# Performance work log

Measured on AMD Instinct MI355X. Metric: run time of the kernel, lower is better.

Reference implementation:

```python
import jax, jax.numpy as jnp
import numpy as np

DIM = 1024
HEADS = 16
DIM_HEAD = 64
INNER = HEADS * DIM_HEAD  # 1024
SCALE = DIM ** (-0.5)  # module scales by dim**-0.5 (not dim_head)


def setup_inputs() -> dict:
    key = jax.random.key(0)
    kx, kqkv, kwo, kbo = jax.random.split(key, 4)
    x = jax.random.normal(kx, (2, 2048, DIM), dtype=jnp.float32)
    W_qkv = jax.random.normal(kqkv, (DIM, 3 * INNER), dtype=jnp.float32) * (DIM ** -0.5)
    W_out = jax.random.normal(kwo, (INNER, DIM), dtype=jnp.float32) * (INNER ** -0.5)
    b_out = jax.random.normal(kbo, (DIM,), dtype=jnp.float32) * 0.01
    return {"x": x, "W_qkv": W_qkv, "W_out": W_out, "b_out": b_out}


def reference(x, W_qkv, W_out, b_out):
    b, n, _ = x.shape
    qkv = x @ W_qkv  # [b, n, 3*inner]
    q, k, v = jnp.split(qkv, 3, axis=-1)
    # [b, n, h*d] -> [b, h, n, d]
    reshape = lambda t: t.reshape(b, n, HEADS, DIM_HEAD).transpose(0, 2, 1, 3)
    q, k, v = reshape(q), reshape(k), reshape(v)
    dots = jnp.einsum('bhid,bhjd->bhij', q, k) * SCALE  # [b, h, n, n]
    attn = jax.nn.softmax(dots, axis=-1)
    out = jnp.einsum('bhij,bhjd->bhid', attn, v)  # [b, h, n, d]
    out = out.transpose(0, 2, 1, 3).reshape(b, n, INNER)
    return out @ W_out + b_out
```

## Files before the change

### kernel.cpp

```cpp
#include <hip/hip_runtime.h>

typedef __bf16 bf16x8 __attribute__((ext_vector_type(8)));
typedef __bf16 bf16x4 __attribute__((ext_vector_type(4)));
typedef __bf16 bf16x2 __attribute__((ext_vector_type(2)));
typedef float f32x4 __attribute__((ext_vector_type(4)));
typedef float f32x16 __attribute__((ext_vector_type(16)));
typedef int i32x4 __attribute__((ext_vector_type(4)));
typedef unsigned int u32x2 __attribute__((ext_vector_type(2)));

__device__ __forceinline__ void async16(void* lds, const void* g) {
  __builtin_amdgcn_global_load_lds(
      (__attribute__((address_space(1))) unsigned int*)(g),
      (__attribute__((address_space(3))) unsigned int*)(lds), 16, 0, 0);
}

__device__ __forceinline__ unsigned int pack2(float a, float b) {
  bf16x2 t;
  t[0] = (__bf16)a;
  t[1] = (__bf16)b;
  return __builtin_bit_cast(unsigned int, t);
}

__device__ __forceinline__ void plswap(unsigned int& d, unsigned int& s) {
#if __has_builtin(__builtin_amdgcn_permlane32_swap)
  u32x2 r = __builtin_amdgcn_permlane32_swap(d, s, false, false);
  d = r[0];
  s = r[1];
#else
  asm("v_permlane32_swap_b32 %0, %1" : "+v"(d), "+v"(s));
#endif
}

__device__ __forceinline__ int detect_block(const unsigned short* win, int* cnt_sh) {
  if (threadIdx.x == 0) *cnt_sh = 0;
  __syncthreads();
  int c = 0;
#pragma unroll
  for (int j = 0; j < 8; j++) {
    const unsigned short u = win[threadIdx.x * 8 + j];
    if (((u >> 7) & 0xFF) >= 0xC0) c++;
  }
  if (c) atomicAdd(cnt_sh, c);
  __syncthreads();
  return (*cnt_sh >= 64) ? 1 : 0;
}

__global__ __launch_bounds__(256) void prep(
    const void* __restrict__ x, const void* __restrict__ Wqkv,
    const void* __restrict__ Wout, __bf16* __restrict__ xb,
    __bf16* __restrict__ WqkvT, __bf16* __restrict__ WoutT,
    int* __restrict__ flagp)
{
  __shared__ __bf16 tile[64 * 65];
  __shared__ int cnt;
  const int bx = blockIdx.x;
  const int t = threadIdx.x;

  if (bx < 2048) {
    const long base = (long)bx * 2048;
    const int f = detect_block((const unsigned short*)x + base, &cnt);
    if (bx == 0 && t == 0) *flagp = f;
    const long i = base + t * 8;
    if (f) {
      const float* s = (const float*)x;
#pragma unroll
      for (int j = 0; j < 8; j++) xb[i + j] = (__bf16)s[i + j];
    } else {
      *(bf16x8*)&xb[i] = *(const bf16x8*)((const __bf16*)x + i);
    }
    return;
  }

  const void* in;  __bf16* out;  int R = 1024, C, tcx, tr;
  if (bx < 2816) {
    const int idx = bx - 2048;
    in = Wqkv; out = WqkvT; C = 3072; tcx = (idx % 48) * 64; tr = (idx / 48) * 64;
  } else {
    const int idx = bx - 2816;
    in = Wout; out = WoutT; C = 1024; tcx = (idx % 16) * 64; tr = (idx / 16) * 64;
  }
  const int f = detect_block((const unsigned short*)in + (long)tr * C + tcx, &cnt);
#pragma unroll
  for (int i = 0; i < 16; i++) {
    const int idx = t + 256 * i;
    const int r = idx >> 6, c = idx & 63;
    const long g = (long)(tr + r) * C + tcx + c;
    tile[r * 65 + c] = f ? (__bf16)((const float*)in)[g] : ((const __bf16*)in)[g];
  }
  __syncthreads();
#pragma unroll
  for (int i = 0; i < 16; i++) {
    const int idx = t + 256 * i;
    const int r = idx >> 6, c = idx & 63;
    out[(long)(tcx + r) * R + tr + c] = tile[c * 65 + r];
  }
}

__global__ __launch_bounds__(256, 3) void gemm_qkv(
    const __bf16* __restrict__ A, const __bf16* __restrict__ Bt,
    __bf16* __restrict__ Cqk, __bf16* __restrict__ Vt)
{
  __shared__ __bf16 smem[17408];
  const int t = threadIdx.x;
  const int l = t & 63;
  const int w = t >> 6;
  const int wr = w >> 1, wc = w & 1;
  const long m0 = (long)blockIdx.x * 128;
  const long n0 = (long)blockIdx.y * 128;
  const int K = 1024;

  const int srow = w * 16 + (l >> 2);
  const int skof = (l & 3) * 8;
  const __bf16* gA = A + (m0 + srow) * (long)K + skof;
  const __bf16* gB = Bt + (n0 + srow) * (long)K + skof;
  const int Ao[2] = {0, 8192}, Bo[2] = {4096, 12288};
  const int lof = w * 512 + l * 8;

  async16(smem + Ao[0] + lof,        gA);
  async16(smem + Ao[0] + 2048 + lof, gA + 64 * (long)K);
  async16(smem + Bo[0] + lof,        gB);
  async16(smem + Bo[0] + 2048 + lof, gB + 64 * (long)K);
  gA += 32; gB += 32;
  __syncthreads();

  f32x4 acc[4][4] = {};

  for (int it = 0; it < 32; it++) {
    if (it < 31) {
      const int nb = (it + 1) & 1;
      async16(smem + Ao[nb] + lof,        gA);
      async16(smem + Ao[nb] + 2048 + lof, gA + 64 * (long)K);
      async16(smem + Bo[nb] + lof,        gB);
      async16(smem + Bo[nb] + 2048 + lof, gB + 64 * (long)K);
      gA += 32; gB += 32;
    }
    const __bf16* As = smem + Ao[it & 1];
    const __bf16* Bs = smem + Bo[it & 1];
    bf16x8 af[4], bfr[4];
#pragma unroll
    for (int mi = 0; mi < 4; mi++)
      af[mi] = *(const bf16x8*)&As[(wr * 64 + mi * 16 + (l & 15)) * 32 + (l >> 4) * 8];
#pragma unroll
    for (int ni = 0; ni < 4; ni++)
      bfr[ni] = *(const bf16x8*)&Bs[(wc * 64 + ni * 16 + (l & 15)) * 32 + (l >> 4) * 8];
#pragma unroll
    for (int mi = 0; mi < 4; mi++)
#pragma unroll
      for (int ni = 0; ni < 4; ni++)
        acc[mi][ni] = __builtin_amdgcn_mfma_f32_16x16x32_bf16(af[mi], bfr[ni], acc[mi][ni], 0, 0, 0);
    __syncthreads();
  }

  if (n0 < 2048) {
#pragma unroll
    for (int mi = 0; mi < 4; mi++)
#pragma unroll
      for (int ni = 0; ni < 4; ni++) {
        const long col = n0 + wc * 64 + ni * 16 + (l & 15);
#pragma unroll
        for (int r = 0; r < 4; r++) {
          const long row = m0 + wr * 64 + mi * 16 + (l >> 4) * 4 + r;
          Cqk[row * 2048 + col] = (__bf16)acc[mi][ni][r];
        }
      }
  } else {
#pragma unroll
    for (int mi = 0; mi < 4; mi++)
#pragma unroll
      for (int ni = 0; ni < 4; ni++) {
        const int c = wc * 64 + ni * 16 + (l & 15);
        const int r = wr * 64 + mi * 16 + (l >> 4) * 4;
        bf16x4 pk;
#pragma unroll
        for (int k = 0; k < 4; k++) pk[k] = (__bf16)acc[mi][ni][k];
        *(bf16x4*)&smem[c * 136 + r] = pk;
      }
    __syncthreads();
    const int b = (int)(m0 >> 11);
    const int nbase = (int)(m0 & 2047);
#pragma unroll
    for (int i = 0; i < 8; i++) {
      const int c = (t >> 4) + i * 16;
      const int r8 = (t & 15) * 8;
      const bf16x8 v = *(const bf16x8*)&smem[c * 136 + r8];
      const int vcol = (int)(n0 - 2048) + c;
      *(bf16x8*)&Vt[((long)(b * 16 + (vcol >> 6)) * 64 + (vcol & 63)) * 2048 + nbase + r8] = v;
    }
  }
}

__global__ __launch_bounds__(256, 2) void gemm_out(
    const __bf16* __restrict__ A, const __bf16* __restrict__ Bt,
    const void* __restrict__ bias_raw, void* __restrict__ C,
    const int* __restrict__ flagp)
{
  __shared__ __bf16 smem[12288];
  const int t = threadIdx.x;
  const int l = t & 63;
  const int w = t >> 6;
  const int wr = w >> 1, wc = w & 1;
  const long m0 = (long)blockIdx.x * 128;
  const long n0 = (long)blockIdx.y * 64;
  const int of = *flagp;
  const int K = 1024;

  const int srow = w * 16 + (l >> 2);
  const int skof = (l & 3) * 8;
  const __bf16* gA = A + (m0 + srow) * (long)K + skof;
  const __bf16* gB = Bt + (n0 + srow) * (long)K + skof;
  const int Ao[2] = {0, 6144}, Bo[2] = {4096, 10240};
  const int lof = w * 512 + l * 8;

  async16(smem + Ao[0] + lof,        gA);
  async16(smem + Ao[0] + 2048 + lof, gA + 64 * (long)K);
  async16(smem + Bo[0] + lof,        gB);
  gA += 32; gB += 32;
  __syncthreads();

  f32x4 acc[4][2] = {};

  for (int it = 0; it < 32; it++) {
    if (it < 31) {
      const int nb = (it + 1) & 1;
      async16(smem + Ao[nb] + lof,        gA);
      async16(smem + Ao[nb] + 2048 + lof, gA + 64 * (long)K);
      async16(smem + Bo[nb] + lof,        gB);
      gA += 32; gB += 32;
    }
    const __bf16* As = smem + Ao[it & 1];
    const __bf16* Bs = smem + Bo[it & 1];
    bf16x8 af[4], bfr[2];
#pragma unroll
    for (int mi = 0; mi < 4; mi++)
      af[mi] = *(const bf16x8*)&As[(wr * 64 + mi * 16 + (l & 15)) * 32 + (l >> 4) * 8];
#pragma unroll
    for (int ni = 0; ni < 2; ni++)
      bfr[ni] = *(const bf16x8*)&Bs[(wc * 32 + ni * 16 + (l & 15)) * 32 + (l >> 4) * 8];
#pragma unroll
    for (int mi = 0; mi < 4; mi++)
#pragma unroll
      for (int ni = 0; ni < 2; ni++)
        acc[mi][ni] = __builtin_amdgcn_mfma_f32_16x16x32_bf16(af[mi], bfr[ni], acc[mi][ni], 0, 0, 0);
    __syncthreads();
  }

#pragma unroll
  for (int mi = 0; mi < 4; mi++)
#pragma unroll
    for (int ni = 0; ni < 2; ni++) {
      const long col = n0 + wc * 32 + ni * 16 + (l & 15);
      const float bv = of ? ((const float*)bias_raw)[col]
                          : (float)((const __bf16*)bias_raw)[col];
#pragma unroll
      for (int r = 0; r < 4; r++) {
        const long row = m0 + wr * 64 + mi * 16 + (l >> 4) * 4 + r;
        const float val = acc[mi][ni][r] + bv;
        const long off = row * 1024 + col;
        if (of) ((float*)C)[off] = val;
        else    ((__bf16*)C)[off] = (__bf16)val;
      }
    }
}

#define EXP2_SCALE 0.045084439f

__global__ __launch_bounds__(256, 4) void attn_kernel(
    const __bf16* __restrict__ qk, const __bf16* __restrict__ Vt,
    __bf16* __restrict__ O)
{
  __shared__ __bf16 smem[16384];
  const int t = threadIdx.x;
  const int l = t & 63;
  const int w = t >> 6;
  const int wi = w & 1, wj = w >> 1;
  const int hl = l >> 5;
  const int i7 = l & 7;
  const int L = blockIdx.y * 32 + blockIdx.x;
  const int bh = (L & 7) * 4 + ((L >> 3) & 3);
  const int qt = L >> 5;
  const int b = bh >> 4, head = bh & 15;
  const long q_row0 = (long)b * 2048 + qt * 64;

  const int srow = w * 8 + (l >> 3);
  const int sdof = ((l & 7) ^ (l >> 3)) * 8;
  const int lof = w * 512 + l * 8;

  const __bf16* gK = qk + ((long)b * 2048 + srow) * 2048 + 1024 + head * 64 + sdof;
  const __bf16* gV = Vt + ((long)bh * 64 + srow) * 2048 + sdof;
  async16(smem + lof,        gK);
  async16(smem + 2048 + lof, gK + 32 * 2048);
  async16(smem + 4096 + lof, gV);
  async16(smem + 6144 + lof, gV + 32 * 2048);
  gK += (long)64 * 2048;
  gV += 64;

  bf16x8 qf[4];
  {
    const __bf16* gQ = qk + (q_row0 + wi * 32 + (l & 31)) * 2048 + head * 64 + hl * 8;
#pragma unroll
    for (int kc = 0; kc < 4; kc++)
      qf[kc] = *(const bf16x8*)(gQ + kc * 16);
  }

  f32x16 accA = {0,0,0,0,0,0,0,0,0,0,0,0,0,0,0,0};
  f32x16 accB = {0,0,0,0,0,0,0,0,0,0,0,0,0,0,0,0};
  float l_i = 0.0f;

  for (int it = 0; it < 32; it++) {
    __syncthreads();
    if (it < 31) {
      const int nb = ((it + 1) & 1) * 8192;
      async16(smem + nb + lof,        gK);
      async16(smem + nb + 2048 + lof, gK + 32 * 2048);
      async16(smem + nb + 4096 + lof, gV);
      async16(smem + nb + 6144 + lof, gV + 32 * 2048);
      gK += (long)64 * 2048;
      gV += 64;
    }
    const __bf16* Ks = smem + (it & 1) * 8192;
    const __bf16* Vs = Ks + 4096;

    f32x16 st = {0,0,0,0,0,0,0,0,0,0,0,0,0,0,0,0};
    __builtin_amdgcn_s_setprio(1);
#pragma unroll
    for (int kc = 0; kc < 4; kc++) {
      const bf16x8 ak = *(const bf16x8*)&Ks[(wj * 32 + (l & 31)) * 64 + (((kc * 2 + hl) ^ i7) * 8)];
      st = __builtin_amdgcn_mfma_f32_32x32x16_bf16(ak, qf[kc], st, 0, 0, 0);
    }
    __builtin_amdgcn_s_setprio(0);

    float rs = 0.0f;
#pragma unroll
    for (int r = 0; r < 16; r++) {
      const float p = exp2f(st[r] * EXP2_SCALE);
      st[r] = p;
      rs += p;
    }
    rs += __shfl_xor(rs, 32, 64);
    l_i += rs;

    unsigned int a0 = pack2(st[0],  st[1]),  b0 = pack2(st[4],  st[5]);
    unsigned int c0 = pack2(st[2],  st[3]),  d0 = pack2(st[6],  st[7]);
    unsigned int a1 = pack2(st[8],  st[9]),  b1 = pack2(st[12], st[13]);
    unsigned int c1 = pack2(st[10], st[11]), d1 = pack2(st[14], st[15]);
    plswap(a0, b0);
    plswap(c0, d0);
    plswap(a1, b1);
    plswap(c1, d1);
    const i32x4 f0 = {(int)a0, (int)c0, (int)b0, (int)d0};
    const i32x4 f1 = {(int)a1, (int)c1, (int)b1, (int)d1};
    const bf16x8 pa0 = __builtin_bit_cast(bf16x8, f0);
    const bf16x8 pa1 = __builtin_bit_cast(bf16x8, f1);

    const int vg = wj * 4;
    const bf16x8 bv00 = *(const bf16x8*)&Vs[((l & 31)) * 64      + (((vg + hl) ^ i7) * 8)];
    const bf16x8 bv01 = *(const bf16x8*)&Vs[(32 + (l & 31)) * 64 + (((vg + hl) ^ i7) * 8)];
    const bf16x8 bv10 = *(const bf16x8*)&Vs[((l & 31)) * 64      + (((vg + 2 + hl) ^ i7) * 8)];
    const bf16x8 bv11 = *(const bf16x8*)&Vs[(32 + (l & 31)) * 64 + (((vg + 2 + hl) ^ i7) * 8)];
    __builtin_amdgcn_s_setprio(1);
    accA = __builtin_amdgcn_mfma_f32_32x32x16_bf16(pa0, bv00, accA, 0, 0, 0);
    accB = __builtin_amdgcn_mfma_f32_32x32x16_bf16(pa0, bv01, accB, 0, 0, 0);
    accA = __builtin_amdgcn_mfma_f32_32x32x16_bf16(pa1, bv10, accA, 0, 0, 0);
    accB = __builtin_amdgcn_mfma_f32_32x32x16_bf16(pa1, bv11, accB, 0, 0, 0);
    __builtin_amdgcn_s_setprio(0);
  }

  __syncthreads();
  float* xbf = (float*)smem;
  float* lb  = (float*)(smem + 8192);
#pragma unroll
  for (int r = 0; r < 16; r++)
    xbf[w * 1024 + r * 64 + l] = wj ? accA[r] : accB[r];
  if (l < 32) lb[w * 32 + l] = l_i;
  __syncthreads();
  const int pw = 2 * (1 - wj) + wi;
#pragma unroll
  for (int r = 0; r < 16; r++) {
    const int iloc = (r & 3) + 8 * (r >> 2) + 4 * hl;
    const float lt = lb[wi * 32 + iloc] + lb[(wi + 2) * 32 + iloc];
    const float own = wj ? accB[r] : accA[r];
    const float o = own + xbf[pw * 1024 + r * 64 + l];
    const long row = q_row0 + wi * 32 + iloc;
    const long col = (long)head * 64 + wj * 32 + (l & 31);
    O[row * 1024 + col] = (__bf16)(o / lt);
  }
}

extern "C" void kernel_launch(void* const* d_in, const int* in_sizes, int n_in,
                              void* d_out, int out_size, void* d_ws, size_t ws_size,
                              hipStream_t stream) {
  const void* x    = d_in[0];
  const void* Wqkv = d_in[1];
  const void* Wout = d_in[2];
  const void* bout = d_in[3];

  char* ws = (char*)d_ws;
  int*    flagp = (int*)ws;
  __bf16* xb    = (__bf16*)(ws + 4096);
  __bf16* Obuf  = xb;
  __bf16* WqkvT = (__bf16*)(ws + 4096 +  8388608);
  __bf16* WoutT = (__bf16*)(ws + 4096 + 14680064);
  __bf16* qkbuf = (__bf16*)(ws + 4096 + 16777216);
  __bf16* VtBuf = (__bf16*)(ws + 4096 + 33554432);

  hipLaunchKernelGGL(prep, dim3(3072), dim3(256), 0, stream,
                     x, Wqkv, Wout, xb, WqkvT, WoutT, flagp);
  hipLaunchKernelGGL(gemm_qkv, dim3(32, 24), dim3(256), 0, stream,
                     xb, WqkvT, qkbuf, VtBuf);
  hipLaunchKernelGGL(attn_kernel, dim3(32, 32), dim3(256), 0, stream,
                     qkbuf, VtBuf, Obuf);
  hipLaunchKernelGGL(gemm_out, dim3(32, 16), dim3(256), 0, stream,
                     Obuf, WoutT, bout, d_out, flagp);
}
```

Before: 200.2 us.

## Software-pipeline PV MFMAs with next QK tile and defer row-sum reduction

The loop is restructured so the P·V MFMAs of iteration i-1 are issued together with the QK MFMAs of iteration i. This lets the softmax exp and pack work overlap with matrix-core work instead of serializing behind it. K fragments are read from LDS before the async prefetch is issued, and V fragments are held in registers for the next iteration. The per-iteration cross-half shuffle of the row sum is replaced by one permlane swap after the loop. The cost is higher register pressure from the extra live P and V fragments, plus an epilogue MFMA block.

```diff
diff --git a/kernel.cpp b/kernel.cpp
--- a/kernel.cpp
+++ b/kernel.cpp
@@ -306,8 +306,22 @@
   f32x16 accB = {0,0,0,0,0,0,0,0,0,0,0,0,0,0,0,0};
   float l_i = 0.0f;
 
+  bf16x8 pa0 = {}, pa1 = {};
+  bf16x8 pvA0 = {}, pvA1 = {}, pvB0 = {}, pvB1 = {};
+
+  const int krow = (wj * 32 + (l & 31)) * 64;
+  const int vg = wj * 4;
+
   for (int it = 0; it < 32; it++) {
     __syncthreads();
+    const __bf16* Ks = smem + (it & 1) * 8192;
+    const __bf16* Vs = Ks + 4096;
+
+    bf16x8 ak[4];
+#pragma unroll
+    for (int kc = 0; kc < 4; kc++)
+      ak[kc] = *(const bf16x8*)&Ks[krow + (((kc * 2 + hl) ^ i7) * 8)];
+
     if (it < 31) {
       const int nb = ((it + 1) & 1) * 8192;
       async16(smem + nb + lof,        gK);
@@ -317,17 +331,24 @@
       gK += (long)64 * 2048;
       gV += 64;
     }
-    const __bf16* Ks = smem + (it & 1) * 8192;
-    const __bf16* Vs = Ks + 4096;
-
+
+    __builtin_amdgcn_s_setprio(1);
+    if (it > 0) {
+      accA = __builtin_amdgcn_mfma_f32_32x32x16_bf16(pa0, pvA0, accA, 0, 0, 0);
+      accB = __builtin_amdgcn_mfma_f32_32x32x16_bf16(pa0, pvB0, accB, 0, 0, 0);
+      accA = __builtin_amdgcn_mfma_f32_32x32x16_bf16(pa1, pvA1, accA, 0, 0, 0);
+      accB = __builtin_amdgcn_mfma_f32_32x32x16_bf16(pa1, pvB1, accB, 0, 0, 0);
+    }
     f32x16 st = {0,0,0,0,0,0,0,0,0,0,0,0,0,0,0,0};
-    __builtin_amdgcn_s_setprio(1);
-#pragma unroll
-    for (int kc = 0; kc < 4; kc++) {
-      const bf16x8 ak = *(const bf16x8*)&Ks[(wj * 32 + (l & 31)) * 64 + (((kc * 2 + hl) ^ i7) * 8)];
-      st = __builtin_amdgcn_mfma_f32_32x32x16_bf16(ak, qf[kc], st, 0, 0, 0);
-    }
+#pragma unroll
+    for (int kc = 0; kc < 4; kc++)
+      st = __builtin_amdgcn_mfma_f32_32x32x16_bf16(ak[kc], qf[kc], st, 0, 0, 0);
     __builtin_amdgcn_s_setprio(0);
+
+    pvA0 = *(const bf16x8*)&Vs[((l & 31)) * 64      + (((vg + hl) ^ i7) * 8)];
+    pvB0 = *(const bf16x8*)&Vs[(32 + (l & 31)) * 64 + (((vg + hl) ^ i7) * 8)];
+    pvA1 = *(const bf16x8*)&Vs[((l & 31)) * 64      + (((vg + 2 + hl) ^ i7) * 8)];
+    pvB1 = *(const bf16x8*)&Vs[(32 + (l & 31)) * 64 + (((vg + 2 + hl) ^ i7) * 8)];
 
     float rs = 0.0f;
 #pragma unroll
@@ -336,7 +357,6 @@
       st[r] = p;
       rs += p;
     }
-    rs += __shfl_xor(rs, 32, 64);
     l_i += rs;
 
     unsigned int a0 = pack2(st[0],  st[1]),  b0 = pack2(st[4],  st[5]);
@@ -349,20 +369,19 @@
     plswap(c1, d1);
     const i32x4 f0 = {(int)a0, (int)c0, (int)b0, (int)d0};
     const i32x4 f1 = {(int)a1, (int)c1, (int)b1, (int)d1};
-    const bf16x8 pa0 = __builtin_bit_cast(bf16x8, f0);
-    const bf16x8 pa1 = __builtin_bit_cast(bf16x8, f1);
-
-    const int vg = wj * 4;
-    const bf16x8 bv00 = *(const bf16x8*)&Vs[((l & 31)) * 64      + (((vg + hl) ^ i7) * 8)];
-    const bf16x8 bv01 = *(const bf16x8*)&Vs[(32 + (l & 31)) * 64 + (((vg + hl) ^ i7) * 8)];
-    const bf16x8 bv10 = *(const bf16x8*)&Vs[((l & 31)) * 64      + (((vg + 2 + hl) ^ i7) * 8)];
-    const bf16x8 bv11 = *(const bf16x8*)&Vs[(32 + (l & 31)) * 64 + (((vg + 2 + hl) ^ i7) * 8)];
-    __builtin_amdgcn_s_setprio(1);
-    accA = __builtin_amdgcn_mfma_f32_32x32x16_bf16(pa0, bv00, accA, 0, 0, 0);
-    accB = __builtin_amdgcn_mfma_f32_32x32x16_bf16(pa0, bv01, accB, 0, 0, 0);
-    accA = __builtin_amdgcn_mfma_f32_32x32x16_bf16(pa1, bv10, accA, 0, 0, 0);
-    accB = __builtin_amdgcn_mfma_f32_32x32x16_bf16(pa1, bv11, accB, 0, 0, 0);
-    __builtin_amdgcn_s_setprio(0);
+    pa0 = __builtin_bit_cast(bf16x8, f0);
+    pa1 = __builtin_bit_cast(bf16x8, f1);
+  }
+
+  accA = __builtin_amdgcn_mfma_f32_32x32x16_bf16(pa0, pvA0, accA, 0, 0, 0);
+  accB = __builtin_amdgcn_mfma_f32_32x32x16_bf16(pa0, pvB0, accB, 0, 0, 0);
+  accA = __builtin_amdgcn_mfma_f32_32x32x16_bf16(pa1, pvA1, accA, 0, 0, 0);
+  accB = __builtin_amdgcn_mfma_f32_32x32x16_bf16(pa1, pvB1, accB, 0, 0, 0);
+
+  {
+    unsigned int a = __builtin_bit_cast(unsigned int, l_i), bswp = a;
+    plswap(a, bswp);
+    l_i = __builtin_bit_cast(float, a) + __builtin_bit_cast(float, bswp);
   }
 
   __syncthreads();
```

After: 200.1 us. No clear change (-0.0%).
